# Optimization experiments

Measured on AMD Instinct MI355X. Metric: run time of the kernel, lower is better.

Reference implementation:

```python
import jax, jax.numpy as jnp
import numpy as np

D = 1024
H = 16
DK = D // H


def apply_rope(x):
    # x: [B, H, T, dk]; interleaved-pair RoPE as in the torch source
    T, dim = x.shape[-2], x.shape[-1]
    inv_freq = 1.0 / (10000.0 ** (jnp.arange(0, dim, 2, dtype=x.dtype) / dim))  # [dk/2]
    pos = jnp.arange(T, dtype=x.dtype)
    sinusoid = pos[:, None] * inv_freq[None, :]  # [T, dk/2]
    sin, cos = jnp.sin(sinusoid), jnp.cos(sinusoid)
    x1, x2 = x[..., ::2], x[..., 1::2]
    rot = jnp.stack([x1 * cos - x2 * sin, x1 * sin + x2 * cos], axis=-1)
    return rot.reshape(x.shape)


def setup_inputs() -> dict:
    key = jax.random.key(0)
    k1, k2, k3, k4, k5 = jax.random.split(key, 5)
    B, T = 2, 2048
    s = 1.0 / np.sqrt(D)
    return {
        "x": jax.random.normal(k1, (B, T, D), dtype=jnp.float32),
        "W_qkv": jax.random.normal(k2, (D, 3 * D), dtype=jnp.float32) * s,
        "b_qkv": jnp.zeros((3 * D,), dtype=jnp.float32),
        "W_out": jax.random.normal(k3, (D, D), dtype=jnp.float32) * s,
        "b_out": jnp.zeros((D,), dtype=jnp.float32),
    }


def reference(x, W_qkv, b_qkv, W_out, b_out):
    B, T, C = x.shape
    qkv = x @ W_qkv + b_qkv  # [B, T, 3D]
    qkv = qkv.reshape(B, T, 3, H, DK).transpose(2, 0, 3, 1, 4)  # [3, B, H, T, dk]
    q, k, v = qkv[0], qkv[1], qkv[2]
    q, k = apply_rope(q), apply_rope(k)
    scores = jnp.einsum("bhtd,bhsd->bhts", q, k) / jnp.sqrt(jnp.asarray(DK, x.dtype))
    causal = jnp.tril(jnp.ones((T, T), dtype=bool))
    scores = jnp.where(causal, scores, jnp.asarray(-1e9, x.dtype))
    probs = jax.nn.softmax(scores, axis=-1)
    attn = jnp.einsum("bhts,bhsd->bhtd", probs, v)  # [B, H, T, dk]
    out = attn.transpose(0, 2, 1, 3).reshape(B, T, C)  # b h t d -> b t (h d)
    return out @ W_out + b_out
```

## Files before the change

kernel.cpp:

```cpp
#include <hip/hip_runtime.h>
#include <math.h>

#define DMODEL 1024
#define NHEAD  16
#define HDK    64
#define BATCH  2
#define SEQ    2048
#define MROWS  (BATCH*SEQ)
#define NQKV   (3*DMODEL)
#define LOG2_10000 13.287712379549449f
#define INV2PI 0.15915494309189535f
#define SCALE_LOG2E 0.1803368801111137f
#define M_FIX 8.0f

typedef __attribute__((ext_vector_type(8))) short bf16x8;
typedef __attribute__((ext_vector_type(4))) float f32x4;

__device__ __forceinline__ short f2bf(float f) {
    union { float f; unsigned u; } v; v.f = f;
    unsigned r = v.u + 0x7fffu + ((v.u >> 16) & 1u);
    return (short)(r >> 16);
}

__device__ __forceinline__ float fast_exp2(float x) {
#if __has_builtin(__builtin_amdgcn_exp2f)
    return __builtin_amdgcn_exp2f(x);
#else
    return exp2f(x);
#endif
}

__device__ __forceinline__ void gld_lds16(const short* g, short* l) {
    __builtin_amdgcn_global_load_lds(
        (const __attribute__((address_space(1))) void*)g,
        (__attribute__((address_space(3))) void*)l, 16, 0, 0);
}

__global__ __launch_bounds__(256) void convert_kernel(
    const float* __restrict__ in, short* __restrict__ out, int n)
{
    int i = (blockIdx.x * 256 + threadIdx.x) * 8;
    if (i >= n) return;
    float4 a = *(const float4*)(in + i);
    float4 b = *(const float4*)(in + i + 4);
    bf16x8 o;
    o[0] = f2bf(a.x); o[1] = f2bf(a.y); o[2] = f2bf(a.z); o[3] = f2bf(a.w);
    o[4] = f2bf(b.x); o[5] = f2bf(b.y); o[6] = f2bf(b.z); o[7] = f2bf(b.w);
    *(bf16x8*)(out + i) = o;
}

__global__ __launch_bounds__(256) void transpose_both_kernel(
    const float* __restrict__ wqkv, const float* __restrict__ wout,
    short* __restrict__ wqkv_t, short* __restrict__ wout_t)
{
    __shared__ short tile[32][33];
    const int tx = threadIdx.x, ty = threadIdx.y;
    int bx = blockIdx.x;
    const float* in; short* out; int N;
    if (bx < 96) { in = wqkv; out = wqkv_t; N = NQKV; }
    else         { in = wout; out = wout_t; N = DMODEL; bx -= 96; }
    const int n0 = bx * 32, k0 = blockIdx.y * 32;
    #pragma unroll
    for (int i = 0; i < 32; i += 8)
        tile[ty + i][tx] = f2bf(in[(size_t)(k0 + ty + i) * N + n0 + tx]);
    __syncthreads();
    #pragma unroll
    for (int i = 0; i < 32; i += 8)
        out[(size_t)(n0 + ty + i) * DMODEL + k0 + tx] = tile[tx][ty + i];
}

__global__ __launch_bounds__(256) void qkv_gemm_kernel(
    const short* __restrict__ xb, const short* __restrict__ Wt,
    const float* __restrict__ bias,
    short* __restrict__ qd, short* __restrict__ kd, short* __restrict__ vtb)
{
    __shared__ __align__(16) short As[128 * 32];
    __shared__ __align__(16) short Bs[128 * 32];
    const int tid = threadIdx.x;
    const int lane = tid & 63, wave = tid >> 6;
    const int wm = wave & 1, wn = wave >> 1;
    const int l15 = lane & 15, quad = lane >> 4;
    const int n0 = blockIdx.x * 128, m0 = blockIdx.y * 128;
    const int srow = lane >> 2, sc = lane & 3;

    const short* gA1 = xb + (size_t)(m0 + wave * 32 + srow) * DMODEL + sc * 8;
    const short* gA2 = gA1 + (size_t)16 * DMODEL;
    const short* gB1 = Wt + (size_t)(n0 + wave * 32 + srow) * DMODEL + sc * 8;
    const short* gB2 = gB1 + (size_t)16 * DMODEL;
    short* lA1 = As + (wave * 32) * 32;
    short* lA2 = As + (wave * 32 + 16) * 32;
    short* lB1 = Bs + (wave * 32) * 32;
    short* lB2 = Bs + (wave * 32 + 16) * 32;

    f32x4 zero = {0.f, 0.f, 0.f, 0.f};
    f32x4 acc[4][4];
    #pragma unroll
    for (int i = 0; i < 4; ++i)
        #pragma unroll
        for (int j = 0; j < 4; ++j) acc[i][j] = zero;

    for (int k0 = 0; k0 < DMODEL; k0 += 32) {
        __syncthreads();
        gld_lds16(gA1 + k0, lA1);
        gld_lds16(gA2 + k0, lA2);
        gld_lds16(gB1 + k0, lB1);
        gld_lds16(gB2 + k0, lB2);
        __syncthreads();
        bf16x8 af[4], bfr[4];
        #pragma unroll
        for (int i = 0; i < 4; ++i)
            af[i] = *(const bf16x8*)&As[(wm * 64 + i * 16 + l15) * 32 + quad * 8];
        #pragma unroll
        for (int j = 0; j < 4; ++j)
            bfr[j] = *(const bf16x8*)&Bs[(wn * 64 + j * 16 + l15) * 32 + quad * 8];
        #pragma unroll
        for (int i = 0; i < 4; ++i)
            #pragma unroll
            for (int j = 0; j < 4; ++j)
                acc[i][j] = __builtin_amdgcn_mfma_f32_16x16x32_bf16(af[i], bfr[j], acc[i][j], 0, 0, 0);
    }

    const int which = n0 >> 10;
    float biasv[4], invf[4];
    int hh[4], dd[4];
    #pragma unroll
    for (int j = 0; j < 4; ++j) {
        const int n = n0 + wn * 64 + j * 16 + l15;
        biasv[j] = bias[n];
        hh[j] = (n & 1023) >> 6;
        dd[j] = n & 63;
        invf[j] = INV2PI * exp2f(-((float)(dd[j] & ~1) / 64.f) * LOG2_10000);
    }
    #pragma unroll
    for (int i = 0; i < 4; ++i) {
        #pragma unroll
        for (int r = 0; r < 4; ++r) {
            const int m = m0 + wm * 64 + i * 16 + quad * 4 + r;
            const int b = m >> 11, t = m & (SEQ - 1);
            #pragma unroll
            for (int j = 0; j < 4; ++j) {
                float val = acc[i][j][r] + biasv[j];
                if (which < 2) {
                    const float rev = (float)t * invf[j];
                    const float fr = rev - floorf(rev);
                    const float s = __builtin_amdgcn_sinf(fr);
                    const float c = __builtin_amdgcn_cosf(fr);
                    const float partner = __shfl_xor(val, 1);
                    val = (lane & 1) ? (partner * s + val * c) : (val * c - partner * s);
                    short* dst = (which == 0) ? qd : kd;
                    dst[((size_t)(b * NHEAD + hh[j]) * SEQ + t) * HDK + dd[j]] = f2bf(val);
                } else {
                    vtb[((size_t)(b * NHEAD + hh[j]) * HDK + dd[j]) * SEQ + t] = f2bf(val);
                }
            }
        }
    }
}

__global__ __launch_bounds__(256) void attn_mfma_kernel(
    const short* __restrict__ qd, const short* __restrict__ kd,
    const short* __restrict__ vt, short* __restrict__ od)
{
    __shared__ __align__(16) short Ks0[64 * 32];
    __shared__ __align__(16) short Ks1[64 * 32];
    __shared__ __align__(16) short Vs0[64 * 32];
    __shared__ __align__(16) short Vs1[64 * 32];
    __shared__ __align__(16) short Ps[4][16][72];
    const int tid = threadIdx.x, lane = tid & 63, w = tid >> 6;
    const int l15 = lane & 15, quad = lane >> 4;
    const int h = blockIdx.y, b = blockIdx.z;
    const size_t base = ((size_t)(b * NHEAD + h)) * SEQ * HDK;
    const int srow = tid >> 2, sc = tid & 3;
    const int lofs = srow * 32 + sc * 8;
    f32x4 zero = {0.f, 0.f, 0.f, 0.f};

    const int qtile[2] = { (int)blockIdx.x, 31 - (int)blockIdx.x };
    const short* kp = kd + base + (size_t)srow * HDK + sc * 8;
    const short* vp = vt + base + (size_t)srow * SEQ + sc * 8;

    #pragma unroll 1
    for (int qi = 0; qi < 2; ++qi) {
        const int q0 = qtile[qi] * 64;
        bf16x8 qf[2];
        {
            const short* qrow = qd + base + (size_t)(q0 + w * 16 + l15) * HDK;
            qf[0] = *(const bf16x8*)(qrow + quad * 8);
            qf[1] = *(const bf16x8*)(qrow + 32 + quad * 8);
        }
        float l_acc[4] = {0.f, 0.f, 0.f, 0.f};
        f32x4 o[4];
        #pragma unroll
        for (int j = 0; j < 4; ++j) o[j] = zero;

        bf16x8 k0v = *(const bf16x8*)kp, k1v = *(const bf16x8*)(kp + 32);
        bf16x8 v0v = *(const bf16x8*)vp, v1v = *(const bf16x8*)(vp + 32);

        const int nkt = q0 / 64 + 1;
        for (int kt = 0; kt < nkt; ++kt) {
            __syncthreads();
            *(bf16x8*)&Ks0[lofs] = k0v; *(bf16x8*)&Ks1[lofs] = k1v;
            *(bf16x8*)&Vs0[lofs] = v0v; *(bf16x8*)&Vs1[lofs] = v1v;
            __syncthreads();
            if (kt + 1 < nkt) {
                const short* kn = kd + base + (size_t)((kt + 1) * 64 + srow) * HDK + sc * 8;
                const short* vn = vt + base + (size_t)srow * SEQ + (kt + 1) * 64 + sc * 8;
                k0v = *(const bf16x8*)kn; k1v = *(const bf16x8*)(kn + 32);
                v0v = *(const bf16x8*)vn; v1v = *(const bf16x8*)(vn + 32);
            } else if (qi == 0) {
                k0v = *(const bf16x8*)kp; k1v = *(const bf16x8*)(kp + 32);
                v0v = *(const bf16x8*)vp; v1v = *(const bf16x8*)(vp + 32);
            }

            f32x4 sacc[4];
            #pragma unroll
            for (int j = 0; j < 4; ++j) {
                bf16x8 kf0 = *(const bf16x8*)&Ks0[(j * 16 + l15) * 32 + quad * 8];
                bf16x8 kf1 = *(const bf16x8*)&Ks1[(j * 16 + l15) * 32 + quad * 8];
                sacc[j] = __builtin_amdgcn_mfma_f32_16x16x32_bf16(qf[0], kf0, zero, 0, 0, 0);
                sacc[j] = __builtin_amdgcn_mfma_f32_16x16x32_bf16(qf[1], kf1, sacc[j], 0, 0, 0);
            }
            if (kt == nkt - 1) {
                const int s0 = kt * 64;
                #pragma unroll
                for (int j = 0; j < 4; ++j) {
                    const int scol = s0 + j * 16 + l15;
                    #pragma unroll
                    for (int r = 0; r < 4; ++r) {
                        const int trow = q0 + w * 16 + quad * 4 + r;
                        const float sv = sacc[j][r] * SCALE_LOG2E - M_FIX;
                        const float p = (scol > trow) ? 0.f : fast_exp2(sv);
                        l_acc[r] += p;
                        Ps[w][quad * 4 + r][j * 16 + l15] = f2bf(p);
                    }
                }
            } else {
                #pragma unroll
                for (int j = 0; j < 4; ++j)
                    #pragma unroll
                    for (int r = 0; r < 4; ++r) {
                        const float p = fast_exp2(sacc[j][r] * SCALE_LOG2E - M_FIX);
                        l_acc[r] += p;
                        Ps[w][quad * 4 + r][j * 16 + l15] = f2bf(p);
                    }
            }
            bf16x8 pf0 = *(const bf16x8*)&Ps[w][l15][quad * 8];
            bf16x8 pf1 = *(const bf16x8*)&Ps[w][l15][32 + quad * 8];
            #pragma unroll
            for (int j = 0; j < 4; ++j) {
                bf16x8 vf0 = *(const bf16x8*)&Vs0[(j * 16 + l15) * 32 + quad * 8];
                bf16x8 vf1 = *(const bf16x8*)&Vs1[(j * 16 + l15) * 32 + quad * 8];
                o[j] = __builtin_amdgcn_mfma_f32_16x16x32_bf16(pf0, vf0, o[j], 0, 0, 0);
                o[j] = __builtin_amdgcn_mfma_f32_16x16x32_bf16(pf1, vf1, o[j], 0, 0, 0);
            }
        }

        #pragma unroll
        for (int r = 0; r < 4; ++r) {
            float sr = l_acc[r];
            #pragma unroll
            for (int off = 1; off < 16; off <<= 1) sr += __shfl_xor(sr, off);
            l_acc[r] = sr;
        }
        #pragma unroll
        for (int r = 0; r < 4; ++r) {
            const float inv = 1.f / l_acc[r];
            const int t = q0 + w * 16 + quad * 4 + r;
            #pragma unroll
            for (int j = 0; j < 4; ++j)
                od[((size_t)(b * SEQ + t) * NHEAD + h) * HDK + j * 16 + l15] =
                    f2bf(o[j][r] * inv);
        }
    }
}

__global__ __launch_bounds__(256) void out_gemm_kernel(
    const short* __restrict__ Ab, const short* __restrict__ Wt,
    const float* __restrict__ bias, float* __restrict__ out)
{
    __shared__ __align__(16) short As[128 * 32];
    __shared__ __align__(16) short Bs[128 * 32];
    const int tid = threadIdx.x;
    const int lane = tid & 63, wave = tid >> 6;
    const int wm = wave & 1, wn = wave >> 1;
    const int l15 = lane & 15, quad = lane >> 4;
    const int n0 = blockIdx.x * 128, m0 = blockIdx.y * 128;
    const int srow = lane >> 2, sc = lane & 3;

    const short* gA1 = Ab + (size_t)(m0 + wave * 32 + srow) * DMODEL + sc * 8;
    const short* gA2 = gA1 + (size_t)16 * DMODEL;
    const short* gB1 = Wt + (size_t)(n0 + wave * 32 + srow) * DMODEL + sc * 8;
    const short* gB2 = gB1 + (size_t)16 * DMODEL;
    short* lA1 = As + (wave * 32) * 32;
    short* lA2 = As + (wave * 32 + 16) * 32;
    short* lB1 = Bs + (wave * 32) * 32;
    short* lB2 = Bs + (wave * 32 + 16) * 32;

    f32x4 zero = {0.f, 0.f, 0.f, 0.f};
    f32x4 acc[4][4];
    #pragma unroll
    for (int i = 0; i < 4; ++i)
        #pragma unroll
        for (int j = 0; j < 4; ++j) acc[i][j] = zero;

    for (int k0 = 0; k0 < DMODEL; k0 += 32) {
        __syncthreads();
        gld_lds16(gA1 + k0, lA1);
        gld_lds16(gA2 + k0, lA2);
        gld_lds16(gB1 + k0, lB1);
        gld_lds16(gB2 + k0, lB2);
        __syncthreads();
        bf16x8 af[4], bfr[4];
        #pragma unroll
        for (int i = 0; i < 4; ++i)
            af[i] = *(const bf16x8*)&As[(wm * 64 + i * 16 + l15) * 32 + quad * 8];
        #pragma unroll
        for (int j = 0; j < 4; ++j)
            bfr[j] = *(const bf16x8*)&Bs[(wn * 64 + j * 16 + l15) * 32 + quad * 8];
        #pragma unroll
        for (int i = 0; i < 4; ++i)
            #pragma unroll
            for (int j = 0; j < 4; ++j)
                acc[i][j] = __builtin_amdgcn_mfma_f32_16x16x32_bf16(af[i], bfr[j], acc[i][j], 0, 0, 0);
    }

    #pragma unroll
    for (int j = 0; j < 4; ++j) {
        const int n = n0 + wn * 64 + j * 16 + l15;
        const float bv = bias[n];
        #pragma unroll
        for (int i = 0; i < 4; ++i)
            #pragma unroll
            for (int r = 0; r < 4; ++r) {
                const int m = m0 + wm * 64 + i * 16 + quad * 4 + r;
                out[(size_t)m * DMODEL + n] = acc[i][j][r] + bv;
            }
    }
}

extern "C" void kernel_launch(void* const* d_in, const int* in_sizes, int n_in,
                              void* d_out, int out_size, void* d_ws, size_t ws_size,
                              hipStream_t stream) {
    const float* x    = (const float*)d_in[0];
    const float* Wqkv = (const float*)d_in[1];
    const float* bqkv = (const float*)d_in[2];
    const float* Wout = (const float*)d_in[3];
    const float* bout = (const float*)d_in[4];
    float* out = (float*)d_out;

    short* ws = (short*)d_ws;
    short* xb     = ws;
    short* wqkv_t = xb + (size_t)4 * 1024 * 1024;
    short* wout_t = wqkv_t + (size_t)3 * 1024 * 1024;
    short* qd     = wout_t + (size_t)1024 * 1024;
    short* kd     = qd + (size_t)4 * 1024 * 1024;
    short* vtb    = kd + (size_t)4 * 1024 * 1024;
    short* attn   = vtb + (size_t)4 * 1024 * 1024;

    convert_kernel<<<(MROWS * DMODEL) / (256 * 8), 256, 0, stream>>>(
        x, xb, MROWS * DMODEL);
    transpose_both_kernel<<<dim3(96 + 32, 32), dim3(32, 8), 0, stream>>>(
        Wqkv, Wout, wqkv_t, wout_t);

    qkv_gemm_kernel<<<dim3(NQKV / 128, MROWS / 128), 256, 0, stream>>>(
        xb, wqkv_t, bqkv, qd, kd, vtb);

    attn_mfma_kernel<<<dim3(16, NHEAD, BATCH), 256, 0, stream>>>(
        qd, kd, vtb, attn);

    out_gemm_kernel<<<dim3(DMODEL / 128, MROWS / 128), 256, 0, stream>>>(
        attn, wout_t, bout, out);
}
```

Measured before the change: 197.8 us.

## Merge prep kernels, pair K/V tiles per sync, and remap attention blocks

The x conversion and the weight transpose kernels are merged into one launch to remove a kernel boundary. The attention kernel now stages two 64-key tiles into LDS per barrier pair, which halves the number of __syncthreads and raises the number of global loads in flight. Its grid is flattened to 1D, with the block index remapped so that blocks with the same query-tile pair but different head/batch are interleaved, which may spread work across XCDs. In exchange the kernel uses more LDS and registers, which can lower occupancy.

```diff
diff --git a/kernel.cpp b/kernel.cpp
--- a/kernel.cpp
+++ b/kernel.cpp
@@ -36,30 +36,31 @@
         (__attribute__((address_space(3))) void*)l, 16, 0, 0);
 }
 
-__global__ __launch_bounds__(256) void convert_kernel(
-    const float* __restrict__ in, short* __restrict__ out, int n)
-{
-    int i = (blockIdx.x * 256 + threadIdx.x) * 8;
-    if (i >= n) return;
-    float4 a = *(const float4*)(in + i);
-    float4 b = *(const float4*)(in + i + 4);
-    bf16x8 o;
-    o[0] = f2bf(a.x); o[1] = f2bf(a.y); o[2] = f2bf(a.z); o[3] = f2bf(a.w);
-    o[4] = f2bf(b.x); o[5] = f2bf(b.y); o[6] = f2bf(b.z); o[7] = f2bf(b.w);
-    *(bf16x8*)(out + i) = o;
-}
-
-__global__ __launch_bounds__(256) void transpose_both_kernel(
-    const float* __restrict__ wqkv, const float* __restrict__ wout,
-    short* __restrict__ wqkv_t, short* __restrict__ wout_t)
+__global__ __launch_bounds__(256) void prep_kernel(
+    const float* __restrict__ x, const float* __restrict__ wqkv,
+    const float* __restrict__ wout,
+    short* __restrict__ xb, short* __restrict__ wqkv_t, short* __restrict__ wout_t)
 {
     __shared__ short tile[32][33];
-    const int tx = threadIdx.x, ty = threadIdx.y;
-    int bx = blockIdx.x;
+    const int tid = threadIdx.x;
+    if (blockIdx.x < 2048) {
+        const int i = (blockIdx.x * 256 + tid) * 8;
+        float4 a = *(const float4*)(x + i);
+        float4 b = *(const float4*)(x + i + 4);
+        bf16x8 o;
+        o[0] = f2bf(a.x); o[1] = f2bf(a.y); o[2] = f2bf(a.z); o[3] = f2bf(a.w);
+        o[4] = f2bf(b.x); o[5] = f2bf(b.y); o[6] = f2bf(b.z); o[7] = f2bf(b.w);
+        *(bf16x8*)(xb + i) = o;
+        return;
+    }
+    const int bx = blockIdx.x - 2048;
+    int nx = bx & 127;
+    const int ky = bx >> 7;
     const float* in; short* out; int N;
-    if (bx < 96) { in = wqkv; out = wqkv_t; N = NQKV; }
-    else         { in = wout; out = wout_t; N = DMODEL; bx -= 96; }
-    const int n0 = bx * 32, k0 = blockIdx.y * 32;
+    if (nx < 96) { in = wqkv; out = wqkv_t; N = NQKV; }
+    else         { in = wout; out = wout_t; N = DMODEL; nx -= 96; }
+    const int tx = tid & 31, ty = tid >> 5;
+    const int n0 = nx * 32, k0 = ky * 32;
     #pragma unroll
     for (int i = 0; i < 32; i += 8)
         tile[ty + i][tx] = f2bf(in[(size_t)(k0 + ty + i) * N + n0 + tx]);
@@ -161,22 +162,26 @@
     const short* __restrict__ qd, const short* __restrict__ kd,
     const short* __restrict__ vt, short* __restrict__ od)
 {
-    __shared__ __align__(16) short Ks0[64 * 32];
-    __shared__ __align__(16) short Ks1[64 * 32];
-    __shared__ __align__(16) short Vs0[64 * 32];
-    __shared__ __align__(16) short Vs1[64 * 32];
+    __shared__ __align__(16) short Ks[2][2][64 * 32];
+    __shared__ __align__(16) short Vs[2][2][64 * 32];
     __shared__ __align__(16) short Ps[4][16][72];
     const int tid = threadIdx.x, lane = tid & 63, w = tid >> 6;
     const int l15 = lane & 15, quad = lane >> 4;
-    const int h = blockIdx.y, b = blockIdx.z;
+    const int id = (int)blockIdx.x;
+    const int c = id & 7, kk = id >> 3;
+    const int qp = kk & 15, jj = kk >> 4;
+    const int hb = c + 8 * jj;
+    const int h = hb & 15, b = hb >> 4;
     const size_t base = ((size_t)(b * NHEAD + h)) * SEQ * HDK;
     const int srow = tid >> 2, sc = tid & 3;
-    const int lofs = srow * 32 + sc * 8;
+    const int lofs = tid * 8;
     f32x4 zero = {0.f, 0.f, 0.f, 0.f};
 
-    const int qtile[2] = { (int)blockIdx.x, 31 - (int)blockIdx.x };
-    const short* kp = kd + base + (size_t)srow * HDK + sc * 8;
-    const short* vp = vt + base + (size_t)srow * SEQ + sc * 8;
+    const int qtile[2] = { qp, 31 - qp };
+    const short* kp0 = kd + base + (size_t)srow * HDK + sc * 8;
+    const short* vp0 = vt + base + (size_t)srow * SEQ + sc * 8;
+    const short* kp1 = kp0 + (size_t)64 * HDK;
+    const short* vp1 = vp0 + 64;
 
     #pragma unroll 1
     for (int qi = 0; qi < 2; ++qi) {
@@ -192,65 +197,84 @@
         #pragma unroll
         for (int j = 0; j < 4; ++j) o[j] = zero;
 
-        bf16x8 k0v = *(const bf16x8*)kp, k1v = *(const bf16x8*)(kp + 32);
-        bf16x8 v0v = *(const bf16x8*)vp, v1v = *(const bf16x8*)(vp + 32);
-
         const int nkt = q0 / 64 + 1;
-        for (int kt = 0; kt < nkt; ++kt) {
+        const int npair = (nkt + 1) >> 1;
+
+        bf16x8 rk[2][2], rv[2][2];
+        rk[0][0] = *(const bf16x8*)kp0; rk[0][1] = *(const bf16x8*)(kp0 + 32);
+        rv[0][0] = *(const bf16x8*)vp0; rv[0][1] = *(const bf16x8*)(vp0 + 32);
+        rk[1][0] = *(const bf16x8*)kp1; rk[1][1] = *(const bf16x8*)(kp1 + 32);
+        rv[1][0] = *(const bf16x8*)vp1; rv[1][1] = *(const bf16x8*)(vp1 + 32);
+
+        for (int p = 0; p < npair; ++p) {
             __syncthreads();
-            *(bf16x8*)&Ks0[lofs] = k0v; *(bf16x8*)&Ks1[lofs] = k1v;
-            *(bf16x8*)&Vs0[lofs] = v0v; *(bf16x8*)&Vs1[lofs] = v1v;
+            *(bf16x8*)&Ks[0][0][lofs] = rk[0][0]; *(bf16x8*)&Ks[0][1][lofs] = rk[0][1];
+            *(bf16x8*)&Vs[0][0][lofs] = rv[0][0]; *(bf16x8*)&Vs[0][1][lofs] = rv[0][1];
+            *(bf16x8*)&Ks[1][0][lofs] = rk[1][0]; *(bf16x8*)&Ks[1][1][lofs] = rk[1][1];
+            *(bf16x8*)&Vs[1][0][lofs] = rv[1][0]; *(bf16x8*)&Vs[1][1][lofs] = rv[1][1];
             __syncthreads();
-            if (kt + 1 < nkt) {
-                const short* kn = kd + base + (size_t)((kt + 1) * 64 + srow) * HDK + sc * 8;
-                const short* vn = vt + base + (size_t)srow * SEQ + (kt + 1) * 64 + sc * 8;
-                k0v = *(const bf16x8*)kn; k1v = *(const bf16x8*)(kn + 32);
-                v0v = *(const bf16x8*)vn; v1v = *(const bf16x8*)(vn + 32);
+            if (p + 1 < npair) {
+                const int sn = (2 * p + 2) * 64;
+                const short* kn = kd + base + (size_t)(sn + srow) * HDK + sc * 8;
+                const short* vn = vt + base + (size_t)srow * SEQ + sn + sc * 8;
+                rk[0][0] = *(const bf16x8*)kn; rk[0][1] = *(const bf16x8*)(kn + 32);
+                rv[0][0] = *(const bf16x8*)vn; rv[0][1] = *(const bf16x8*)(vn + 32);
+                const short* kn2 = kn + (size_t)64 * HDK;
+                const short* vn2 = vn + 64;
+                rk[1][0] = *(const bf16x8*)kn2; rk[1][1] = *(const bf16x8*)(kn2 + 32);
+                rv[1][0] = *(const bf16x8*)vn2; rv[1][1] = *(const bf16x8*)(vn2 + 32);
             } else if (qi == 0) {
-                k0v = *(const bf16x8*)kp; k1v = *(const bf16x8*)(kp + 32);
-                v0v = *(const bf16x8*)vp; v1v = *(const bf16x8*)(vp + 32);
+                rk[0][0] = *(const bf16x8*)kp0; rk[0][1] = *(const bf16x8*)(kp0 + 32);
+                rv[0][0] = *(const bf16x8*)vp0; rv[0][1] = *(const bf16x8*)(vp0 + 32);
+                rk[1][0] = *(const bf16x8*)kp1; rk[1][1] = *(const bf16x8*)(kp1 + 32);
+                rv[1][0] = *(const bf16x8*)vp1; rv[1][1] = *(const bf16x8*)(vp1 + 32);
             }
 
-            f32x4 sacc[4];
-            #pragma unroll
-            for (int j = 0; j < 4; ++j) {
-                bf16x8 kf0 = *(const bf16x8*)&Ks0[(j * 16 + l15) * 32 + quad * 8];
-                bf16x8 kf1 = *(const bf16x8*)&Ks1[(j * 16 + l15) * 32 + quad * 8];
-                sacc[j] = __builtin_amdgcn_mfma_f32_16x16x32_bf16(qf[0], kf0, zero, 0, 0, 0);
-                sacc[j] = __builtin_amdgcn_mfma_f32_16x16x32_bf16(qf[1], kf1, sacc[j], 0, 0, 0);
-            }
-            if (kt == nkt - 1) {
-                const int s0 = kt * 64;
+            #pragma unroll
+            for (int tt = 0; tt < 2; ++tt) {
+                const int kt = 2 * p + tt;
+                if (tt == 1 && kt >= nkt) break;
+                f32x4 sacc[4];
                 #pragma unroll
                 for (int j = 0; j < 4; ++j) {
-                    const int scol = s0 + j * 16 + l15;
+                    bf16x8 kf0 = *(const bf16x8*)&Ks[tt][0][(j * 16 + l15) * 32 + quad * 8];
+                    bf16x8 kf1 = *(const bf16x8*)&Ks[tt][1][(j * 16 + l15) * 32 + quad * 8];
+                    sacc[j] = __builtin_amdgcn_mfma_f32_16x16x32_bf16(qf[0], kf0, zero, 0, 0, 0);
+                    sacc[j] = __builtin_amdgcn_mfma_f32_16x16x32_bf16(qf[1], kf1, sacc[j], 0, 0, 0);
+                }
+                if (kt == nkt - 1) {
+                    const int s0 = kt * 64;
                     #pragma unroll
-                    for (int r = 0; r < 4; ++r) {
-                        const int trow = q0 + w * 16 + quad * 4 + r;
-                        const float sv = sacc[j][r] * SCALE_LOG2E - M_FIX;
-                        const float p = (scol > trow) ? 0.f : fast_exp2(sv);
-                        l_acc[r] += p;
-                        Ps[w][quad * 4 + r][j * 16 + l15] = f2bf(p);
+                    for (int j = 0; j < 4; ++j) {
+                        const int scol = s0 + j * 16 + l15;
+                        #pragma unroll
+                        for (int r = 0; r < 4; ++r) {
+                            const int trow = q0 + w * 16 + quad * 4 + r;
+                            const float sv = sacc[j][r] * SCALE_LOG2E - M_FIX;
+                            const float pv = (scol > trow) ? 0.f : fast_exp2(sv);
+                            l_acc[r] += pv;
+                            Ps[w][quad * 4 + r][j * 16 + l15] = f2bf(pv);
+                        }
                     }
+                } else {
+                    #pragma unroll
+                    for (int j = 0; j < 4; ++j)
+                        #pragma unroll
+                        for (int r = 0; r < 4; ++r) {
+                            const float pv = fast_exp2(sacc[j][r] * SCALE_LOG2E - M_FIX);
+                            l_acc[r] += pv;
+                            Ps[w][quad * 4 + r][j * 16 + l15] = f2bf(pv);
+                        }
                 }
-            } else {
+                bf16x8 pf0 = *(const bf16x8*)&Ps[w][l15][quad * 8];
+                bf16x8 pf1 = *(const bf16x8*)&Ps[w][l15][32 + quad * 8];
                 #pragma unroll
-                for (int j = 0; j < 4; ++j)
-                    #pragma unroll
-                    for (int r = 0; r < 4; ++r) {
-                        const float p = fast_exp2(sacc[j][r] * SCALE_LOG2E - M_FIX);
-                        l_acc[r] += p;
-                        Ps[w][quad * 4 + r][j * 16 + l15] = f2bf(p);
-                    }
-            }
-            bf16x8 pf0 = *(const bf16x8*)&Ps[w][l15][quad * 8];
-            bf16x8 pf1 = *(const bf16x8*)&Ps[w][l15][32 + quad * 8];
-            #pragma unroll
-            for (int j = 0; j < 4; ++j) {
-                bf16x8 vf0 = *(const bf16x8*)&Vs0[(j * 16 + l15) * 32 + quad * 8];
-                bf16x8 vf1 = *(const bf16x8*)&Vs1[(j * 16 + l15) * 32 + quad * 8];
-                o[j] = __builtin_amdgcn_mfma_f32_16x16x32_bf16(pf0, vf0, o[j], 0, 0, 0);
-                o[j] = __builtin_amdgcn_mfma_f32_16x16x32_bf16(pf1, vf1, o[j], 0, 0, 0);
+                for (int j = 0; j < 4; ++j) {
+                    bf16x8 vf0 = *(const bf16x8*)&Vs[tt][0][(j * 16 + l15) * 32 + quad * 8];
+                    bf16x8 vf1 = *(const bf16x8*)&Vs[tt][1][(j * 16 + l15) * 32 + quad * 8];
+                    o[j] = __builtin_amdgcn_mfma_f32_16x16x32_bf16(pf0, vf0, o[j], 0, 0, 0);
+                    o[j] = __builtin_amdgcn_mfma_f32_16x16x32_bf16(pf1, vf1, o[j], 0, 0, 0);
+                }
             }
         }
 
@@ -356,16 +380,12 @@
     short* vtb    = kd + (size_t)4 * 1024 * 1024;
     short* attn   = vtb + (size_t)4 * 1024 * 1024;
 
-    convert_kernel<<<(MROWS * DMODEL) / (256 * 8), 256, 0, stream>>>(
-        x, xb, MROWS * DMODEL);
-    transpose_both_kernel<<<dim3(96 + 32, 32), dim3(32, 8), 0, stream>>>(
-        Wqkv, Wout, wqkv_t, wout_t);
+    prep_kernel<<<2048 + 4096, 256, 0, stream>>>(x, Wqkv, Wout, xb, wqkv_t, wout_t);
 
     qkv_gemm_kernel<<<dim3(NQKV / 128, MROWS / 128), 256, 0, stream>>>(
         xb, wqkv_t, bqkv, qd, kd, vtb);
 
-    attn_mfma_kernel<<<dim3(16, NHEAD, BATCH), 256, 0, stream>>>(
-        qd, kd, vtb, attn);
+    attn_mfma_kernel<<<512, 256, 0, stream>>>(qd, kd, vtb, attn);
 
     out_gemm_kernel<<<dim3(DMODEL / 128, MROWS / 128), 256, 0, stream>>>(
         attn, wout_t, bout, out);
```

After: 196.0 us. No clear change (-0.9%).
